# Optimization experiments

Measured on AMD Instinct MI355X. Metric: run time of the kernel, lower is better.

## Reference

```python
import jax, jax.numpy as jnp
import numpy as np

N_NODES = 100000
N_EDGES = 1600000
IN, HID, OUT = 128, 128, 64


def setup_inputs() -> dict:
    key = jax.random.key(0)
    ks = jax.random.split(key, 12)
    x = jax.random.normal(ks[0], (N_NODES, IN), dtype=jnp.float32)
    src = jax.random.randint(ks[1], (N_EDGES,), 0, N_NODES, dtype=jnp.int32)
    dst = jax.random.randint(ks[2], (N_EDGES,), 0, N_NODES, dtype=jnp.int32)

    def lin(k, fan_in, fan_out):
        return jax.random.normal(k, (fan_in, fan_out), dtype=jnp.float32) / jnp.sqrt(jnp.float32(fan_in))

    return {
        "x": x, "src": src, "dst": dst,
        "w_self_0": lin(ks[3], IN, HID), "w_neigh_0": lin(ks[4], IN, HID), "b_0": jnp.zeros((HID,), jnp.float32),
        "w_self_1": lin(ks[5], HID, HID), "w_neigh_1": lin(ks[6], HID, HID), "b_1": jnp.zeros((HID,), jnp.float32),
        "w_self_2": lin(ks[7], HID, OUT), "w_neigh_2": lin(ks[8], HID, OUT), "b_2": jnp.zeros((OUT,), jnp.float32),
    }


def reference(x, src, dst, w_self_0, w_neigh_0, b_0, w_self_1, w_neigh_1, b_1, w_self_2, w_neigh_2, b_2):
    n = x.shape[0]
    # in-degree per dst node; zero-degree nodes keep aggregated 0 (clamp avoids div-by-0)
    deg = jax.ops.segment_sum(jnp.ones_like(dst, dtype=x.dtype), dst, num_segments=n)
    inv_deg = (1.0 / jnp.maximum(deg, 1.0))[:, None]

    def sage_layer(h, w_s, w_n, b):
        # irregular gather of src features, segment-mean over dst
        agg = jax.ops.segment_sum(h[src], dst, num_segments=n) * inv_deg
        return h @ w_s + agg @ w_n + b

    h = jax.nn.relu(sage_layer(x, w_self_0, w_neigh_0, b_0))   # dropout = identity (eval)
    h = jax.nn.relu(sage_layer(h, w_self_1, w_neigh_1, b_1))
    return sage_layer(h, w_self_2, w_neigh_2, b_2)
```

## Files before the change

### kernel.cpp

```cpp
#include <hip/hip_runtime.h>


#define NN 100000
#define NE 1600000
#define BSH 7
#define BND 128
#define NB  782
#define NBLKS 256
#define EPB ((NE + NBLKS - 1) / NBLKS)
#define STOT (NB * NBLKS)
#define SCAN_E 2048
#define NSB ((STOT + SCAN_E - 1) / SCAN_E)
#define GEMM0_BLOCKS 782

typedef __attribute__((ext_vector_type(8))) short short8;
typedef __attribute__((ext_vector_type(4))) float f32x4;
typedef unsigned int uint;
typedef unsigned short ushort;

__device__ inline ushort f2bf(float f) {
    uint u = __float_as_uint(f);
    u += 0x7FFFu + ((u >> 16) & 1u);
    return (ushort)(u >> 16);
}
__device__ inline float bf_lo(uint w) { return __uint_as_float(w << 16); }
__device__ inline float bf_hi(uint w) { return __uint_as_float(w & 0xFFFF0000u); }

template<int NCS, int NCN, bool XF32, bool ABF>
__device__ void gemm_body(int wid, int tid,
    const void* __restrict__ Hv, const short8* __restrict__ wp,
    const float* __restrict__ bias, void* __restrict__ Av, ushort* __restrict__ Bt)
{
    constexpr int NCT = (NCS + NCN) / 16;
    if (wid >= NN / 16) return;
    const int lane = tid & 63;
    const int m = lane & 15;
    const int q = lane >> 4;

    short8 af[4];
    if (XF32) {
        const float* hp = (const float*)Hv + (size_t)(wid * 16 + m) * 128;
        #pragma unroll
        for (int kt = 0; kt < 4; ++kt) {
            const float4 f0 = *(const float4*)(hp + kt * 32 + q * 8);
            const float4 f1 = *(const float4*)(hp + kt * 32 + q * 8 + 4);
            short8 v;
            v[0] = (short)f2bf(f0.x); v[1] = (short)f2bf(f0.y);
            v[2] = (short)f2bf(f0.z); v[3] = (short)f2bf(f0.w);
            v[4] = (short)f2bf(f1.x); v[5] = (short)f2bf(f1.y);
            v[6] = (short)f2bf(f1.z); v[7] = (short)f2bf(f1.w);
            af[kt] = v;
        }
    } else {
        const short8* hp = (const short8*)((const ushort*)Hv + (size_t)(wid * 16 + m) * 128);
        #pragma unroll
        for (int kt = 0; kt < 4; ++kt) af[kt] = hp[kt * 4 + q];
    }

    f32x4 acc[NCT];
    #pragma unroll
    for (int i = 0; i < NCT; ++i) acc[i] = (f32x4){0.f, 0.f, 0.f, 0.f};

    #pragma unroll
    for (int ct = 0; ct < NCT; ++ct) {
        #pragma unroll
        for (int kt = 0; kt < 4; ++kt) {
            const short8 bf = wp[(ct * 4 + kt) * 64 + lane];
            acc[ct] = __builtin_amdgcn_mfma_f32_16x16x32_bf16(af[kt], bf, acc[ct], 0, 0, 0);
        }
    }

    const int r0 = wid * 16 + q * 4;
    #pragma unroll
    for (int ct = 0; ct < NCS / 16; ++ct) {
        const int c = ct * 16 + m;
        const float bv = bias[c];
        #pragma unroll
        for (int r = 0; r < 4; ++r) {
            const float v = acc[ct][r] + bv;
            if (ABF) ((ushort*)Av)[(size_t)(r0 + r) * NCS + c] = f2bf(v);
            else     ((float*) Av)[(size_t)(r0 + r) * NCS + c] = v;
        }
    }
    #pragma unroll
    for (int ct = NCS / 16; ct < NCT; ++ct) {
        const int c = ct * 16 + m - NCS;
        #pragma unroll
        for (int r = 0; r < 4; ++r)
            Bt[(size_t)(r0 + r) * NCN + c] = f2bf(acc[ct][r]);
    }
}

template<int NCS, int NCN, bool XF32, bool ABF>
__global__ __launch_bounds__(512) void gemm_mfma_k(
    const void* __restrict__ Hv, const ushort* __restrict__ Wf,
    const float* __restrict__ bias, void* __restrict__ Av, ushort* __restrict__ Bt)
{
    constexpr int NCT = (NCS + NCN) / 16;
    __shared__ short8 wl[NCT * 4 * 64];
    uint4* dl = (uint4*)wl;
    const uint4* sg = (const uint4*)Wf;
    for (int i = threadIdx.x; i < NCT * 4 * 64; i += 512) dl[i] = sg[i];
    __syncthreads();
    gemm_body<NCS, NCN, XF32, ABF>(
        (blockIdx.x * 512 + threadIdx.x) >> 6, threadIdx.x, Hv, wl, bias, Av, Bt);
}

__global__ __launch_bounds__(256) void phist_pack_k(
    const int* __restrict__ dst, int* __restrict__ histG,
    const float* __restrict__ ws0, const float* __restrict__ wn0, ushort* __restrict__ wf0,
    const float* __restrict__ ws1, const float* __restrict__ wn1, ushort* __restrict__ wf1,
    const float* __restrict__ ws2, const float* __restrict__ wn2, ushort* __restrict__ wf2)
{
    __shared__ int h[NB];
    const int t = threadIdx.x;
    if (blockIdx.x < NBLKS) {
        for (int i = t; i < NB; i += 256) h[i] = 0;
        __syncthreads();
        const int blk = blockIdx.x;
        const int e0 = blk * EPB;
        const int e1 = min(e0 + EPB, NE);
        for (int e = e0 + t; e < e1; e += 256)
            atomicAdd(&h[dst[e] >> BSH], 1);
        __syncthreads();
        for (int i = t; i < NB; i += 256)
            histG[i * NBLKS + blk] = h[i];
        return;
    }
    const int b = blockIdx.x - NBLKS;
    const float *ws, *wn; ushort* wf; int ncs, idx;
    if (b < 16)      { ws = ws0; wn = wn0; wf = wf0; ncs = 128; idx = b * 256 + t; }
    else if (b < 32) { ws = ws1; wn = wn1; wf = wf1; ncs = 128; idx = (b - 16) * 256 + t; }
    else             { ws = ws2; wn = wn2; wf = wf2; ncs = 64;  idx = (b - 32) * 256 + t; }
    const int total = (2 * ncs / 16) * 4 * 64;
    if (idx >= total) return;
    const int l = idx & 63;
    const int f = idx >> 6;
    const int kt = f & 3;
    const int ct = f >> 2;
    const int n = ct * 16 + (l & 15);
    const int k0 = kt * 32 + (l >> 4) * 8;
    uint w[4];
    #pragma unroll
    for (int p = 0; p < 4; ++p) {
        const int k = k0 + p * 2;
        float v0, v1;
        if (n < ncs) { v0 = ws[k * ncs + n];         v1 = ws[(k + 1) * ncs + n]; }
        else         { v0 = wn[k * ncs + (n - ncs)]; v1 = wn[(k + 1) * ncs + (n - ncs)]; }
        w[p] = (uint)f2bf(v0) | ((uint)f2bf(v1) << 16);
    }
    uint4 o; o.x = w[0]; o.y = w[1]; o.z = w[2]; o.w = w[3];
    ((uint4*)wf)[idx] = o;
}

__global__ __launch_bounds__(256) void scan1_k(int* __restrict__ data, int* __restrict__ blksum) {
    __shared__ int lds[256];
    const int t = threadIdx.x;
    const int base = blockIdx.x * SCAN_E + t * 8;
    int v[8];
    int s = 0;
    #pragma unroll
    for (int i = 0; i < 8; ++i) {
        const int idx = base + i;
        v[i] = (idx < STOT) ? data[idx] : 0;
        s += v[i];
    }
    lds[t] = s;
    __syncthreads();
    #pragma unroll
    for (int off = 1; off < 256; off <<= 1) {
        const int cur = lds[t];
        const int y = (t >= off) ? lds[t - off] : 0;
        __syncthreads();
        lds[t] = cur + y;
        __syncthreads();
    }
    const int incl = lds[t];
    if (t == 255) blksum[blockIdx.x] = incl;
    int run = incl - s;
    #pragma unroll
    for (int i = 0; i < 8; ++i) {
        const int idx = base + i;
        if (idx < STOT) data[idx] = run;
        run += v[i];
    }
}

__global__ __launch_bounds__(256) void scan3_k(int* __restrict__ data, const int* __restrict__ blksum) {
    __shared__ int lds[256];
    const int t = threadIdx.x;
    lds[t] = (t < NSB) ? blksum[t] : 0;
    __syncthreads();
    #pragma unroll
    for (int off = 1; off < 256; off <<= 1) {
        const int cur = lds[t];
        const int y = (t >= off) ? lds[t - off] : 0;
        __syncthreads();
        lds[t] = cur + y;
        __syncthreads();
    }
    const int add = (blockIdx.x == 0) ? 0 : lds[blockIdx.x - 1];
    const int base = blockIdx.x * SCAN_E + t * 8;
    #pragma unroll
    for (int i = 0; i < 8; ++i) {
        const int idx = base + i;
        if (idx < STOT) data[idx] += add;
    }
}

__global__ __launch_bounds__(512) void pscatter_gemm0_k(
    const int* __restrict__ src, const int* __restrict__ dst,
    const int* __restrict__ histG, int* __restrict__ pb,
    const float* __restrict__ x, const ushort* __restrict__ wf0,
    const float* __restrict__ b0, ushort* __restrict__ Abf, ushort* __restrict__ Bt)
{
    __shared__ uint4 sh[4096];
    const int t = threadIdx.x;
    if (blockIdx.x < NBLKS) {
        int* wc = (int*)sh;
        const int blk = blockIdx.x;
        for (int i = t; i < NB; i += 512) wc[i] = histG[i * NBLKS + blk];
        __syncthreads();
        const int e0 = blk * EPB;
        const int e1 = min(e0 + EPB, NE);
        for (int e = e0 + t; e < e1; e += 512) {
            const int d = dst[e];
            const int pos = atomicAdd(&wc[d >> BSH], 1);
            pb[pos] = (src[e] << BSH) | (d & (BND - 1));
        }
        return;
    }
    const uint4* sg = (const uint4*)wf0;
    for (int i = t; i < 4096; i += 512) sh[i] = sg[i];
    __syncthreads();
    gemm_body<128, 128, true, true>(
        ((blockIdx.x - NBLKS) * 512 + t) >> 6, t, x, (const short8*)sh, b0, Abf, Bt);
}

__global__ __launch_bounds__(256) void bucket_place_k(const int* __restrict__ histG,
                                                      const int* __restrict__ pb,
                                                      int* __restrict__ row,
                                                      int* __restrict__ esrc) {
    __shared__ int cnt[BND], wc[BND], excl[BND], scan[BND];
    const int b = blockIdx.x;
    const int t = threadIdx.x;
    if (t < BND) { cnt[t] = 0; wc[t] = 0; }
    __syncthreads();
    const int s0 = histG[b * NBLKS];
    const int s1 = (b + 1 < NB) ? histG[(b + 1) * NBLKS] : NE;
    for (int e = s0 + t; e < s1; e += 256)
        atomicAdd(&cnt[pb[e] & (BND - 1)], 1);
    __syncthreads();
    if (t < BND) scan[t] = cnt[t];
    __syncthreads();
    for (int off = 1; off < BND; off <<= 1) {
        int nv = 0;
        if (t < BND) {
            nv = scan[t];
            if (t >= off) nv += scan[t - off];
        }
        __syncthreads();
        if (t < BND) scan[t] = nv;
        __syncthreads();
    }
    if (t < BND) {
        const int ex = scan[t] - cnt[t];
        excl[t] = ex;
        const int node = b * BND + t;
        if (node <= NN) row[node] = s0 + ex;
    }
    __syncthreads();
    for (int e = s0 + t; e < s1; e += 256) {
        const int p = pb[e];
        const int dl = p & (BND - 1);
        const int pos = s0 + excl[dl] + atomicAdd(&wc[dl], 1);
        esrc[pos] = p >> BSH;
    }
}

__global__ __launch_bounds__(256) void agg128_k(
    const int* __restrict__ row, const int* __restrict__ esrc,
    const ushort* __restrict__ Bt, const ushort* __restrict__ Abf, ushort* __restrict__ Hb)
{
    const int w = (blockIdx.x * 256 + threadIdx.x) >> 6;
    const int half = (threadIdx.x >> 5) & 1;
    const int ln = threadIdx.x & 31;
    const int node = w * 2 + half;
    if (node >= NN) return;
    const int e0 = row[node];
    const int e1 = row[node + 1];
    const uint2* B = (const uint2*)Bt;
    float a0 = 0.f, a1 = 0.f, a2 = 0.f, a3 = 0.f;
    int e = e0;
    for (; e + 8 <= e1; e += 8) {
        int s[8];
        #pragma unroll
        for (int j = 0; j < 8; ++j) s[j] = esrc[e + j];
        uint2 v[8];
        #pragma unroll
        for (int j = 0; j < 8; ++j) v[j] = B[(size_t)s[j] * 32 + ln];
        #pragma unroll
        for (int j = 0; j < 8; ++j) {
            a0 += bf_lo(v[j].x); a1 += bf_hi(v[j].x);
            a2 += bf_lo(v[j].y); a3 += bf_hi(v[j].y);
        }
    }
    for (; e + 2 <= e1; e += 2) {
        const int s0 = esrc[e], s1 = esrc[e + 1];
        const uint2 v0 = B[(size_t)s0 * 32 + ln];
        const uint2 v1 = B[(size_t)s1 * 32 + ln];
        a0 += bf_lo(v0.x) + bf_lo(v1.x); a1 += bf_hi(v0.x) + bf_hi(v1.x);
        a2 += bf_lo(v0.y) + bf_lo(v1.y); a3 += bf_hi(v0.y) + bf_hi(v1.y);
    }
    if (e < e1) {
        const uint2 v = B[(size_t)esrc[e] * 32 + ln];
        a0 += bf_lo(v.x); a1 += bf_hi(v.x);
        a2 += bf_lo(v.y); a3 += bf_hi(v.y);
    }
    const int deg = e1 - e0;
    const float invd = (deg > 0) ? 1.0f / (float)deg : 0.0f;
    const uint2 aw = ((const uint2*)Abf)[(size_t)node * 32 + ln];
    const float v0 = fmaxf(bf_lo(aw.x) + a0 * invd, 0.f);
    const float v1 = fmaxf(bf_hi(aw.x) + a1 * invd, 0.f);
    const float v2 = fmaxf(bf_lo(aw.y) + a2 * invd, 0.f);
    const float v3 = fmaxf(bf_hi(aw.y) + a3 * invd, 0.f);
    uint2 o;
    o.x = (uint)f2bf(v0) | ((uint)f2bf(v1) << 16);
    o.y = (uint)f2bf(v2) | ((uint)f2bf(v3) << 16);
    ((uint2*)Hb)[(size_t)node * 32 + ln] = o;
}

__global__ __launch_bounds__(256) void agg64_k(
    const int* __restrict__ row, const int* __restrict__ esrc,
    const ushort* __restrict__ Bt, float* __restrict__ out)
{
    const int node = (blockIdx.x * 256 + threadIdx.x) >> 4;
    const int ln = threadIdx.x & 15;
    if (node >= NN) return;
    const int e0 = row[node];
    const int e1 = row[node + 1];
    const uint2* B = (const uint2*)Bt;
    float a0 = 0.f, a1 = 0.f, a2 = 0.f, a3 = 0.f;
    int e = e0;
    for (; e + 8 <= e1; e += 8) {
        int s[8];
        #pragma unroll
        for (int j = 0; j < 8; ++j) s[j] = esrc[e + j];
        uint2 v[8];
        #pragma unroll
        for (int j = 0; j < 8; ++j) v[j] = B[(size_t)s[j] * 16 + ln];
        #pragma unroll
        for (int j = 0; j < 8; ++j) {
            a0 += bf_lo(v[j].x); a1 += bf_hi(v[j].x);
            a2 += bf_lo(v[j].y); a3 += bf_hi(v[j].y);
        }
    }
    for (; e + 2 <= e1; e += 2) {
        const int s0 = esrc[e], s1 = esrc[e + 1];
        const uint2 v0 = B[(size_t)s0 * 16 + ln];
        const uint2 v1 = B[(size_t)s1 * 16 + ln];
        a0 += bf_lo(v0.x) + bf_lo(v1.x); a1 += bf_hi(v0.x) + bf_hi(v1.x);
        a2 += bf_lo(v0.y) + bf_lo(v1.y); a3 += bf_hi(v0.y) + bf_hi(v1.y);
    }
    if (e < e1) {
        const uint2 v = B[(size_t)esrc[e] * 16 + ln];
        a0 += bf_lo(v.x); a1 += bf_hi(v.x);
        a2 += bf_lo(v.y); a3 += bf_hi(v.y);
    }
    const int deg = e1 - e0;
    const float invd = (deg > 0) ? 1.0f / (float)deg : 0.0f;
    float4* op = (float4*)(out + (size_t)node * 64 + ln * 4);
    float4 o = *op;
    o.x += a0 * invd; o.y += a1 * invd;
    o.z += a2 * invd; o.w += a3 * invd;
    *op = o;
}

__device__ inline float4 relu4f(float4 v) {
    v.x = fmaxf(v.x, 0.f); v.y = fmaxf(v.y, 0.f);
    v.z = fmaxf(v.z, 0.f); v.w = fmaxf(v.w, 0.f);
    return v;
}
template<int NCOL, bool RELU_IN, bool BIAS>
__global__ __launch_bounds__(256) void gemm_k(
    const float* in, const float* __restrict__ W,
    const float* __restrict__ bias, float* out)
{
    constexpr int K = 128;
    constexpr int QUADS = NCOL / 4;
    constexpr int G = 256 / QUADS;
    constexpr int RPT = 32 / G;
    __shared__ float Wlds[K * NCOL];
    {
        const float4* Wg = reinterpret_cast<const float4*>(W);
        float4* Wl = reinterpret_cast<float4*>(Wlds);
        #pragma unroll
        for (int i = 0; i < K * NCOL / 4 / 256; ++i)
            Wl[threadIdx.x + i * 256] = Wg[threadIdx.x + i * 256];
    }
    __syncthreads();
    const int tx = threadIdx.x % QUADS;
    const int ty = threadIdx.x / QUADS;
    const int row0 = blockIdx.x * 32;
    const float* rp[RPT];
    #pragma unroll
    for (int i = 0; i < RPT; ++i) rp[i] = in + (size_t)(row0 + ty + i * G) * K;
    float acc[RPT][4];
    #pragma unroll
    for (int i = 0; i < RPT; ++i) acc[i][0] = acc[i][1] = acc[i][2] = acc[i][3] = 0.f;
    #pragma unroll 2
    for (int kc = 0; kc < K; kc += 4) {
        float4 h4[RPT];
        #pragma unroll
        for (int i = 0; i < RPT; ++i) {
            h4[i] = *reinterpret_cast<const float4*>(rp[i] + kc);
            if (RELU_IN) h4[i] = relu4f(h4[i]);
        }
        #pragma unroll
        for (int kk = 0; kk < 4; ++kk) {
            const float4 w4 = *reinterpret_cast<const float4*>(&Wlds[(kc + kk) * NCOL + tx * 4]);
            #pragma unroll
            for (int i = 0; i < RPT; ++i) {
                const float hv = (&h4[i].x)[kk];
                acc[i][0] = fmaf(hv, w4.x, acc[i][0]);
                acc[i][1] = fmaf(hv, w4.y, acc[i][1]);
                acc[i][2] = fmaf(hv, w4.z, acc[i][2]);
                acc[i][3] = fmaf(hv, w4.w, acc[i][3]);
            }
        }
    }
    float4 b4 = make_float4(0.f, 0.f, 0.f, 0.f);
    if (BIAS) b4 = *reinterpret_cast<const float4*>(&bias[tx * 4]);
    #pragma unroll
    for (int i = 0; i < RPT; ++i) {
        const int r = row0 + ty + i * G;
        float4 o;
        o.x = acc[i][0] + b4.x; o.y = acc[i][1] + b4.y;
        o.z = acc[i][2] + b4.z; o.w = acc[i][3] + b4.w;
        *reinterpret_cast<float4*>(&out[(size_t)r * NCOL + tx * 4]) = o;
    }
}
__global__ void deg_k(const int* __restrict__ dst, float* __restrict__ deg, int E) {
    const int i = blockIdx.x * blockDim.x + threadIdx.x;
    if (i < E) atomicAdd(&deg[dst[i]], 1.0f);
}
__global__ void inv_k(float* deg, int n) {
    const int i = blockIdx.x * blockDim.x + threadIdx.x;
    if (i < n) deg[i] = 1.0f / fmaxf(deg[i], 1.0f);
}
__global__ __launch_bounds__(256) void scatter128_k(
    const int* __restrict__ src, const int* __restrict__ dst,
    const float* __restrict__ inv, const float* __restrict__ B, float* A, int E) {
    const int lane = threadIdx.x & 63;
    int w = (blockIdx.x * 256 + threadIdx.x) >> 6;
    const int nw = (gridDim.x * 256) >> 6;
    for (int e = w; e < E; e += nw) {
        const int s = src[e], d = dst[e];
        const float sc = inv[d];
        const float2 v = *reinterpret_cast<const float2*>(&B[(size_t)s * 128 + lane * 2]);
        atomicAdd(&A[(size_t)d * 128 + lane * 2    ], v.x * sc);
        atomicAdd(&A[(size_t)d * 128 + lane * 2 + 1], v.y * sc);
    }
}
__global__ __launch_bounds__(256) void scatter64_k(
    const int* __restrict__ src, const int* __restrict__ dst,
    const float* __restrict__ inv, const float* __restrict__ B, float* A, int E) {
    const int lane = threadIdx.x & 63;
    int w = (blockIdx.x * 256 + threadIdx.x) >> 6;
    const int nw = (gridDim.x * 256) >> 6;
    for (int e = w; e < E; e += nw) {
        const int s = src[e], d = dst[e];
        atomicAdd(&A[(size_t)d * 64 + lane], B[(size_t)s * 64 + lane] * inv[d]);
    }
}

extern "C" void kernel_launch(void* const* d_in, const int* in_sizes, int n_in,
                              void* d_out, int out_size, void* d_ws, size_t ws_size,
                              hipStream_t stream) {
    const float* x   = (const float*)d_in[0];
    const int*   src = (const int*)  d_in[1];
    const int*   dst = (const int*)  d_in[2];
    const float* ws0 = (const float*)d_in[3];
    const float* wn0 = (const float*)d_in[4];
    const float* b0  = (const float*)d_in[5];
    const float* ws1 = (const float*)d_in[6];
    const float* wn1 = (const float*)d_in[7];
    const float* b1  = (const float*)d_in[8];
    const float* ws2 = (const float*)d_in[9];
    const float* wn2 = (const float*)d_in[10];
    const float* b2  = (const float*)d_in[11];
    float* out = (float*)d_out;

    const size_t O_BLK  = 4096;
    const size_t O_ROW  = 16384;
    const size_t O_WF0  = 417792;
    const size_t O_WF1  = 483328;
    const size_t O_WF2  = 548864;
    const size_t O_ESRC = 581632;
    const size_t O_PB   = 6983680;
    const size_t O_A    = 14286848;
    const size_t O_BT   = 39890944;
    const size_t O_HB   = 65495040;
    const size_t NEED   = 91095040;

    if (ws_size >= NEED) {
        int*    blks  = (int*)   ((char*)d_ws + O_BLK);
        int*    row   = (int*)   ((char*)d_ws + O_ROW);
        ushort* wf0   = (ushort*)((char*)d_ws + O_WF0);
        ushort* wf1   = (ushort*)((char*)d_ws + O_WF1);
        ushort* wf2   = (ushort*)((char*)d_ws + O_WF2);
        int*    esrc  = (int*)   ((char*)d_ws + O_ESRC);
        int*    pb    = (int*)   ((char*)d_ws + O_PB);
        ushort* Abf   = (ushort*)((char*)d_ws + O_A);
        ushort* Bt    = (ushort*)((char*)d_ws + O_BT);
        ushort* Hb    = (ushort*)((char*)d_ws + O_HB);
        int*    histG = (int*)   ((char*)d_ws + O_HB);

        phist_pack_k<<<NBLKS + 40, 256, 0, stream>>>(dst, histG,
            ws0, wn0, wf0, ws1, wn1, wf1, ws2, wn2, wf2);
        scan1_k<<<NSB, 256, 0, stream>>>(histG, blks);
        scan3_k<<<NSB, 256, 0, stream>>>(histG, blks);
        pscatter_gemm0_k<<<NBLKS + GEMM0_BLOCKS, 512, 0, stream>>>(
            src, dst, histG, pb, x, wf0, b0, Abf, Bt);
        bucket_place_k<<<NB, 256, 0, stream>>>(histG, pb, row, esrc);

        const int AGG128_BLOCKS = (NN / 2 + 3) / 4;
        const int A64B = (NN + 15) / 16;
        const int GEMM512_BLOCKS = (NN / 16 + 7) / 8;

        agg128_k<<<AGG128_BLOCKS, 256, 0, stream>>>(row, esrc, Bt, Abf, Hb);
        gemm_mfma_k<128, 128, false, true ><<<GEMM512_BLOCKS, 512, 0, stream>>>(Hb, wf1, b1, Abf, Bt);
        agg128_k<<<AGG128_BLOCKS, 256, 0, stream>>>(row, esrc, Bt, Abf, Hb);
        gemm_mfma_k<64, 64, false, false><<<GEMM512_BLOCKS, 512, 0, stream>>>(Hb, wf2, b2, out, Bt);
        agg64_k<<<A64B, 256, 0, stream>>>(row, esrc, Bt, out);
    } else {
        float* inv = (float*)d_ws;
        float* H0  = (float*)((char*)d_ws + (1u << 20));
        float* Bf  = H0 + (size_t)NN * 128;
        const int GB = NN / 32;
        const int SC_BLOCKS = 4096;
        hipMemsetAsync(inv, 0, NN * sizeof(float), stream);
        deg_k<<<(NE + 255) / 256, 256, 0, stream>>>(dst, inv, NE);
        inv_k<<<(NN + 255) / 256, 256, 0, stream>>>(inv, NN);
        gemm_k<128, false, false><<<GB, 256, 0, stream>>>(x, wn0, nullptr, Bf);
        gemm_k<128, false, true ><<<GB, 256, 0, stream>>>(x, ws0, b0, H0);
        scatter128_k<<<SC_BLOCKS, 256, 0, stream>>>(src, dst, inv, Bf, H0, NE);
        gemm_k<128, true, false><<<GB, 256, 0, stream>>>(H0, wn1, nullptr, Bf);
        gemm_k<128, true, true ><<<GB, 256, 0, stream>>>(H0, ws1, b1, H0);
        scatter128_k<<<SC_BLOCKS, 256, 0, stream>>>(src, dst, inv, Bf, H0, NE);
        gemm_k<64, true, false><<<GB, 256, 0, stream>>>(H0, wn2, nullptr, Bf);
        gemm_k<64, true, true ><<<GB, 256, 0, stream>>>(H0, ws2, b2, out);
        scatter64_k<<<SC_BLOCKS, 256, 0, stream>>>(src, dst, inv, Bf, out, NE);
    }
}
```

Baseline: 360.1 us.

## Move gemm0 to run alongside bucket placement and vectorize edge reads

The partition scatter becomes its own kernel, and the layer-0 GEMM blocks now share a launch with the per-bucket placement work instead of with the scatter. Bucket placement runs with 512 threads and keeps up to six packed edges per thread in registers, so pb is read once rather than twice. The histogram and scatter loops read dst and src as int2 pairs. These int2 loops assume EPB is even and that each block's edge range is aligned, which holds for the fixed sizes. Each bucket thread also carries more registers.

```diff
diff --git a/kernel.cpp b/kernel.cpp
--- a/kernel.cpp
+++ b/kernel.cpp
@@ -12,6 +12,7 @@
 #define SCAN_E 2048
 #define NSB ((STOT + SCAN_E - 1) / SCAN_E)
 #define GEMM0_BLOCKS 782
+#define KMAX 6
 
 typedef __attribute__((ext_vector_type(8))) short short8;
 typedef __attribute__((ext_vector_type(4))) float f32x4;
@@ -119,9 +120,12 @@
         __syncthreads();
         const int blk = blockIdx.x;
         const int e0 = blk * EPB;
-        const int e1 = min(e0 + EPB, NE);
-        for (int e = e0 + t; e < e1; e += 256)
-            atomicAdd(&h[dst[e] >> BSH], 1);
+        const int2* dp = (const int2*)(dst + e0);
+        for (int k = t; k < EPB / 2; k += 256) {
+            const int2 d2 = dp[k];
+            atomicAdd(&h[d2.x >> BSH], 1);
+            atomicAdd(&h[d2.y >> BSH], 1);
+        }
         __syncthreads();
         for (int i = t; i < NB; i += 256)
             histG[i * NBLKS + blk] = h[i];
@@ -208,25 +212,99 @@
     }
 }
 
-__global__ __launch_bounds__(512) void pscatter_gemm0_k(
+__global__ __launch_bounds__(512) void pscatter_k(
     const int* __restrict__ src, const int* __restrict__ dst,
-    const int* __restrict__ histG, int* __restrict__ pb,
+    const int* __restrict__ histG, int* __restrict__ pb)
+{
+    __shared__ int wc[NB];
+    const int t = threadIdx.x;
+    const int blk = blockIdx.x;
+    for (int i = t; i < NB; i += 512) wc[i] = histG[i * NBLKS + blk];
+    __syncthreads();
+    const int e0 = blk * EPB;
+    const int2* dp = (const int2*)(dst + e0);
+    const int2* sp = (const int2*)(src + e0);
+    for (int k = t; k < EPB / 2; k += 512) {
+        const int2 d2 = dp[k];
+        const int2 s2 = sp[k];
+        const int p0 = atomicAdd(&wc[d2.x >> BSH], 1);
+        pb[p0] = (s2.x << BSH) | (d2.x & (BND - 1));
+        const int p1 = atomicAdd(&wc[d2.y >> BSH], 1);
+        pb[p1] = (s2.y << BSH) | (d2.y & (BND - 1));
+    }
+}
+
+__global__ __launch_bounds__(512) void bucketgemm0_k(
+    const int* __restrict__ histG, const int* __restrict__ pb,
+    int* __restrict__ row, int* __restrict__ esrc,
     const float* __restrict__ x, const ushort* __restrict__ wf0,
     const float* __restrict__ b0, ushort* __restrict__ Abf, ushort* __restrict__ Bt)
 {
     __shared__ uint4 sh[4096];
     const int t = threadIdx.x;
-    if (blockIdx.x < NBLKS) {
-        int* wc = (int*)sh;
-        const int blk = blockIdx.x;
-        for (int i = t; i < NB; i += 512) wc[i] = histG[i * NBLKS + blk];
-        __syncthreads();
-        const int e0 = blk * EPB;
-        const int e1 = min(e0 + EPB, NE);
-        for (int e = e0 + t; e < e1; e += 512) {
-            const int d = dst[e];
-            const int pos = atomicAdd(&wc[d >> BSH], 1);
-            pb[pos] = (src[e] << BSH) | (d & (BND - 1));
+    if (blockIdx.x < NB) {
+        int* cnt  = (int*)sh;
+        int* wc   = cnt + BND;
+        int* excl = wc + BND;
+        int* scn  = excl + BND;
+        const int b = blockIdx.x;
+        if (t < BND) { cnt[t] = 0; wc[t] = 0; }
+        __syncthreads();
+        const int s0 = histG[b * NBLKS];
+        const int s1 = (b + 1 < NB) ? histG[(b + 1) * NBLKS] : NE;
+        const int n = s1 - s0;
+        int held[KMAX];
+        const bool fits = (n <= KMAX * 512);
+        if (fits) {
+            #pragma unroll
+            for (int i = 0; i < KMAX; ++i) {
+                const int e = s0 + t + i * 512;
+                held[i] = (e < s1) ? pb[e] : -1;
+            }
+            #pragma unroll
+            for (int i = 0; i < KMAX; ++i)
+                if (held[i] >= 0) atomicAdd(&cnt[held[i] & (BND - 1)], 1);
+        } else {
+            for (int e = s0 + t; e < s1; e += 512)
+                atomicAdd(&cnt[pb[e] & (BND - 1)], 1);
+        }
+        __syncthreads();
+        if (t < BND) scn[t] = cnt[t];
+        __syncthreads();
+        for (int off = 1; off < BND; off <<= 1) {
+            int nv = 0;
+            if (t < BND) {
+                nv = scn[t];
+                if (t >= off) nv += scn[t - off];
+            }
+            __syncthreads();
+            if (t < BND) scn[t] = nv;
+            __syncthreads();
+        }
+        if (t < BND) {
+            const int ex = scn[t] - cnt[t];
+            excl[t] = ex;
+            const int node = b * BND + t;
+            if (node <= NN) row[node] = s0 + ex;
+        }
+        __syncthreads();
+        if (fits) {
+            #pragma unroll
+            for (int i = 0; i < KMAX; ++i) {
+                if (held[i] >= 0) {
+                    const int p = held[i];
+                    const int dl = p & (BND - 1);
+                    const int pos = s0 + excl[dl] + atomicAdd(&wc[dl], 1);
+                    esrc[pos] = p >> BSH;
+                }
+            }
+        } else {
+            for (int e = s0 + t; e < s1; e += 512) {
+                const int p = pb[e];
+                const int dl = p & (BND - 1);
+                const int pos = s0 + excl[dl] + atomicAdd(&wc[dl], 1);
+                esrc[pos] = p >> BSH;
+            }
         }
         return;
     }
@@ -234,48 +312,7 @@
     for (int i = t; i < 4096; i += 512) sh[i] = sg[i];
     __syncthreads();
     gemm_body<128, 128, true, true>(
-        ((blockIdx.x - NBLKS) * 512 + t) >> 6, t, x, (const short8*)sh, b0, Abf, Bt);
-}
-
-__global__ __launch_bounds__(256) void bucket_place_k(const int* __restrict__ histG,
-                                                      const int* __restrict__ pb,
-                                                      int* __restrict__ row,
-                                                      int* __restrict__ esrc) {
-    __shared__ int cnt[BND], wc[BND], excl[BND], scan[BND];
-    const int b = blockIdx.x;
-    const int t = threadIdx.x;
-    if (t < BND) { cnt[t] = 0; wc[t] = 0; }
-    __syncthreads();
-    const int s0 = histG[b * NBLKS];
-    const int s1 = (b + 1 < NB) ? histG[(b + 1) * NBLKS] : NE;
-    for (int e = s0 + t; e < s1; e += 256)
-        atomicAdd(&cnt[pb[e] & (BND - 1)], 1);
-    __syncthreads();
-    if (t < BND) scan[t] = cnt[t];
-    __syncthreads();
-    for (int off = 1; off < BND; off <<= 1) {
-        int nv = 0;
-        if (t < BND) {
-            nv = scan[t];
-            if (t >= off) nv += scan[t - off];
-        }
-        __syncthreads();
-        if (t < BND) scan[t] = nv;
-        __syncthreads();
-    }
-    if (t < BND) {
-        const int ex = scan[t] - cnt[t];
-        excl[t] = ex;
-        const int node = b * BND + t;
-        if (node <= NN) row[node] = s0 + ex;
-    }
-    __syncthreads();
-    for (int e = s0 + t; e < s1; e += 256) {
-        const int p = pb[e];
-        const int dl = p & (BND - 1);
-        const int pos = s0 + excl[dl] + atomicAdd(&wc[dl], 1);
-        esrc[pos] = p >> BSH;
-    }
+        ((blockIdx.x - NB) * 512 + t) >> 6, t, x, (const short8*)sh, b0, Abf, Bt);
 }
 
 __global__ __launch_bounds__(256) void agg128_k(
@@ -520,9 +557,9 @@
             ws0, wn0, wf0, ws1, wn1, wf1, ws2, wn2, wf2);
         scan1_k<<<NSB, 256, 0, stream>>>(histG, blks);
         scan3_k<<<NSB, 256, 0, stream>>>(histG, blks);
-        pscatter_gemm0_k<<<NBLKS + GEMM0_BLOCKS, 512, 0, stream>>>(
-            src, dst, histG, pb, x, wf0, b0, Abf, Bt);
-        bucket_place_k<<<NB, 256, 0, stream>>>(histG, pb, row, esrc);
+        pscatter_k<<<NBLKS, 512, 0, stream>>>(src, dst, histG, pb);
+        bucketgemm0_k<<<NB + GEMM0_BLOCKS, 512, 0, stream>>>(
+            histG, pb, row, esrc, x, wf0, b0, Abf, Bt);
 
         const int AGG128_BLOCKS = (NN / 2 + 3) / 4;
         const int A64B = (NN + 15) / 16;
```

New measurement: 353.2 us. Within noise of the previous version (-1.9%).
